# Performance work log

Hardware: AMD Instinct MI355X
Metric: run time of the kernel (lower is better)

The kernel has to match this reference:

```python
import math
import jax, jax.numpy as jnp
import numpy as np
from jax import lax

LEAKY_SLOPE = 0.2
ACT_GAIN = math.sqrt(2.0)

def bilinear_filter():
    h = jnp.array([1.0, 3.0, 3.0, 1.0], dtype=jnp.float32)
    h = h[:, None] * h[None, :]
    return h / jnp.sum(h)

def setup_inputs() -> dict:
    key = jax.random.key(0)
    ks = jax.random.split(key, 6)
    B, Cin, Cout, W_DIM, R = 16, 512, 512, 512, 64
    return {
        "x": jax.random.normal(ks[0], (B, Cin, R // 2, R // 2), dtype=jnp.float32),
        "w": jax.random.normal(ks[1], (B, W_DIM), dtype=jnp.float32),
        "noise_raw": jax.random.normal(ks[2], (B, 1, R, R), dtype=jnp.float32),
        "affine_weight": jax.random.normal(ks[3], (Cin, W_DIM), dtype=jnp.float32),
        "affine_bias": jnp.ones((Cin,), dtype=jnp.float32),
        "weight": jax.random.normal(ks[4], (Cout, Cin, 3, 3), dtype=jnp.float32),
        "bias": 0.1 * jax.random.normal(ks[5], (Cout,), dtype=jnp.float32),
        "noise_strength": jnp.float32(1.0),
    }

def reference(x, w, noise_raw, affine_weight, affine_bias, weight, bias, noise_strength):
    B, Cin = x.shape[0], x.shape[1]
    Cout = weight.shape[0]
    w_dim = affine_weight.shape[1]
    # EqualizedLinear affine: weight_gain = 1/sqrt(in), bias_gain = 1, no activation
    styles = w @ (affine_weight * (1.0 / math.sqrt(w_dim))).T + affine_bias  # [B, Cin]
    # demodulation coefficients from modulated weights
    wmod = weight[None] * styles[:, None, :, None, None]                      # [B,Cout,Cin,3,3]
    dcoefs = lax.rsqrt(jnp.sum(jnp.square(wmod), axis=(2, 3, 4)) + 1e-8)     # [B, Cout]
    # modulate input instead of weights
    xs = x * styles[:, :, None, None]
    # up=True path: conv_transpose2d(x, weight.transpose(0,1), stride=2, padding=0)
    # == dilated conv with spatially flipped kernel, pad k-1=2
    w_flip = weight[:, :, ::-1, ::-1]
    y = lax.conv_general_dilated(
        xs, w_flip, window_strides=(1, 1), padding=[(2, 2), (2, 2)],
        lhs_dilation=(2, 2), dimension_numbers=("NCHW", "OIHW", "NCHW"))    # [B,Cout,2H+1,2H+1]
    # filter2d with 4x4 bilinear kernel, gain=4, padding=1 (depthwise)
    f = bilinear_filter() * 4.0
    kd = jnp.tile(f[None, None], (Cout, 1, 1, 1))                            # [Cout,1,4,4]
    y = lax.conv_general_dilated(
        y, kd, window_strides=(1, 1), padding=[(1, 1), (1, 1)],
        dimension_numbers=("NCHW", "OIHW", "NCHW"), feature_group_count=Cout)  # [B,Cout,2H,2H]
    # addcmul: noise + y * dcoefs
    noise = noise_raw * noise_strength
    y = noise + y * dcoefs[:, :, None, None]
    # bias, act gain sqrt(2), leaky relu 0.2
    y = (y + bias[None, :, None, None]) * ACT_GAIN
    return jnp.where(y >= 0, y, LEAKY_SLOPE * y)
```

## Files before the change

### kernel.cpp

```cpp
#include <hip/hip_runtime.h>
#include <hip/hip_bf16.h>
#include <stdint.h>

typedef float f32x4 __attribute__((ext_vector_type(4)));
typedef __bf16 bf16x8 __attribute__((ext_vector_type(8)));

#define GLDS16(gp, lp) __builtin_amdgcn_global_load_lds( \
    (const __attribute__((address_space(1))) void*)(gp), \
    (__attribute__((address_space(3))) void*)(lp), 16, 0, 0)

static __device__ __forceinline__ unsigned short f2bf(float f) {
    unsigned int u = __float_as_uint(f);
    u = (u + 0x7fffu + ((u >> 16) & 1u)) >> 16;
    return (unsigned short)u;
}
static __device__ __forceinline__ float bf2f(unsigned short v) {
    return __uint_as_float(((unsigned int)v) << 16);
}

#define O_STYLES 0
#define O_DCOEF  32768
#define O_XS     65536
#define O_WP     19005440
#define O_Y1     23724032
#define O_WSQ    23724032
#define WS_NEED  96075776
#define SP 1104

__global__ __launch_bounds__(256) void k_styles(const float* __restrict__ w,
                                                const float* __restrict__ aw,
                                                const float* __restrict__ ab,
                                                float* __restrict__ styles) {
    int g = blockIdx.x * 256 + threadIdx.x;
    int b = g >> 9, ci = g & 511;
    const float4* wr = (const float4*)(w + b * 512);
    const float4* ar = (const float4*)(aw + ci * 512);
    float acc = 0.f;
    for (int k = 0; k < 128; ++k) {
        float4 wv = wr[k], av = ar[k];
        acc += wv.x * av.x + wv.y * av.y + wv.z * av.z + wv.w * av.w;
    }
    styles[g] = acc * 0.04419417382415922f + ab[ci];
}

__global__ __launch_bounds__(256) void k_wprep(const float* __restrict__ weight,
                                               float* __restrict__ wsq,
                                               unsigned short* __restrict__ wp) {
    int g = blockIdx.x * 256 + threadIdx.x;
    const float* wb = weight + (long)g * 9;
    float v[9]; float s = 0.f;
#pragma unroll
    for (int t = 0; t < 9; ++t) { v[t] = wb[t]; s += v[t] * v[t]; }
    wsq[g] = s;
    const int wri[9] = {2, 2, 0, 0, 2, 0, 1, 1, 1};
    const int wci[9] = {2, 0, 2, 0, 1, 1, 2, 0, 1};
#pragma unroll
    for (int t = 0; t < 9; ++t)
        wp[t * 262144 + g] = f2bf(v[wri[t] * 3 + wci[t]]);
}

__global__ __launch_bounds__(256) void k_dcoef(const float* __restrict__ styles,
                                               const float* __restrict__ wsq,
                                               float* __restrict__ dcoefs) {
    int g = blockIdx.x * 256 + threadIdx.x;
    int b = g >> 9, co = g & 511;
    const float4* sr = (const float4*)(styles + b * 512);
    const float4* qr = (const float4*)(wsq + co * 512);
    float acc = 1e-8f;
    for (int k = 0; k < 128; ++k) {
        float4 sv = sr[k], qv = qr[k];
        acc += sv.x * sv.x * qv.x + sv.y * sv.y * qv.y + sv.z * sv.z * qv.z + sv.w * sv.w * qv.w;
    }
    dcoefs[g] = rsqrtf(acc);
}

__global__ __launch_bounds__(256) void k_xprep(const float* __restrict__ x,
                                               const float* __restrict__ styles,
                                               unsigned short* __restrict__ xs) {
    __shared__ float T[128][33];
    int bid = blockIdx.x;
    int cc = bid & 3, i = (bid >> 2) & 31, b = bid >> 7;
    int t = threadIdx.x;
    int ci0 = cc * 128;
    int j_r = t & 31, cl_r = t >> 5;
    const float* xp = x + (((long)(b * 512 + ci0)) * 32 + i) * 32;
#pragma unroll
    for (int it = 0; it < 16; ++it) {
        int cl = cl_r + it * 8;
        T[cl][j_r] = xp[cl * 1024 + j_r];
    }
    __syncthreads();
    int ci_w = t & 127, jg = t >> 7;
    float sv = styles[b * 512 + ci0 + ci_w];
    unsigned short* op = xs + (((long)(b * 34 + (i + 1))) * 34 + 1) * 512 + ci0 + ci_w;
#pragma unroll
    for (int jj = 0; jj < 16; ++jj) {
        int j = jg * 16 + jj;
        op[(long)j * 512] = f2bf(T[ci_w][j] * sv);
    }
}

__global__ __launch_bounds__(256) void k_conv(const unsigned short* __restrict__ xs,
                                              const unsigned short* __restrict__ wp,
                                              unsigned short* __restrict__ y1) {
    __shared__ __align__(16) unsigned char lds[16384];
    int bid = (blockIdx.x & 7) * 288 + (blockIdx.x >> 3);
    int nt = bid & 3;
    int tmp = bid >> 2;
    int mt = tmp % 9;
    int tmp2 = tmp / 9;
    int par = tmp2 & 3, b = tmp2 >> 2;
    int tid = threadIdx.x;
    int wave = tid >> 6, lane = tid & 63;

    const int coff = (tid & 3) * 16;
    long abase0, abase1, bbase0, bbase1;
    {
        int row0 = tid >> 2;
        int gm0 = mt * 128 + row0;
        int r0 = gm0 / 33, s0 = gm0 % 33; if (r0 > 32) r0 = 32;
        int gm1 = gm0 + 64;
        int r1 = gm1 / 33, s1 = gm1 % 33; if (r1 > 32) r1 = 32;
        abase0 = (long)(((b * 34 + r0) * 34 + s0)) * 1024 + coff;
        abase1 = (long)(((b * 34 + r1) * 34 + s1)) * 1024 + coff;
        int co0 = nt * 128 + row0;
        bbase0 = (long)co0 * 1024 + coff;
        bbase1 = (long)(co0 + 64) * 1024 + coff;
    }
    const unsigned char* xsb = (const unsigned char*)xs;
    const unsigned char* wpb = (const unsigned char*)wp;

    int a_par = par >> 1, c_par = par & 1;
    int ntaps = a_par ? (c_par ? 1 : 2) : (c_par ? 2 : 4);
    int tapofs = (par == 0) ? 0 : ((par == 1) ? 4 : ((par == 2) ? 6 : 8));
    int KT = ntaps << 4;

    f32x4 acc[4][4];
#pragma unroll
    for (int mi = 0; mi < 4; ++mi)
#pragma unroll
        for (int ni = 0; ni < 4; ++ni)
            acc[mi][ni] = (f32x4){0.f, 0.f, 0.f, 0.f};

    int wr = wave >> 1, wc = wave & 1;
    int lrow = lane & 15;
    int lk = (lane >> 4) * 16;

    for (int kt = 0; kt < KT; ++kt) {
        int tl = kt >> 4, cib = kt & 15;
        int dio = a_par ? 1 : (c_par ? tl : (tl >> 1));
        int djo = c_par ? 1 : (a_par ? tl : (tl & 1));
        long dd = (long)dio * 34816 + (long)djo * 1024 + cib * 64;
        long wd = (long)(tapofs + tl) * 524288 + cib * 64;
        GLDS16(xsb + abase0 + dd, lds + wave * 1024);
        GLDS16(xsb + abase1 + dd, lds + 4096 + wave * 1024);
        GLDS16(wpb + bbase0 + wd, lds + 8192 + wave * 1024);
        GLDS16(wpb + bbase1 + wd, lds + 12288 + wave * 1024);
        __syncthreads();
        bf16x8 af[4], bfr[4];
#pragma unroll
        for (int mi = 0; mi < 4; ++mi)
            af[mi] = *(const bf16x8*)(lds + (wr * 64 + mi * 16 + lrow) * 64 + lk);
#pragma unroll
        for (int ni = 0; ni < 4; ++ni)
            bfr[ni] = *(const bf16x8*)(lds + 8192 + (wc * 64 + ni * 16 + lrow) * 64 + lk);
#pragma unroll
        for (int mi = 0; mi < 4; ++mi)
#pragma unroll
            for (int ni = 0; ni < 4; ++ni)
                acc[mi][ni] = __builtin_amdgcn_mfma_f32_16x16x32_bf16(af[mi], bfr[ni], acc[mi][ni], 0, 0, 0);
        __syncthreads();
    }

    long plane = (long)(b * 4 + par) * 512;
#pragma unroll
    for (int mi = 0; mi < 4; ++mi) {
        int gm0 = mt * 128 + wr * 64 + mi * 16 + (lane >> 4) * 4;
#pragma unroll
        for (int ni = 0; ni < 4; ++ni) {
            int co = nt * 128 + wc * 64 + ni * 16 + (lane & 15);
            unsigned short* dst = y1 + (plane + co) * SP + gm0;
            if (gm0 <= 1084) {
                ushort4 pk;
                pk.x = f2bf(acc[mi][ni][0]);
                pk.y = f2bf(acc[mi][ni][1]);
                pk.z = f2bf(acc[mi][ni][2]);
                pk.w = f2bf(acc[mi][ni][3]);
                *(ushort4*)dst = pk;
            } else if (gm0 == 1088) {
                dst[0] = f2bf(acc[mi][ni][0]);
            }
        }
    }
}

__global__ __launch_bounds__(256) void k_blur(const unsigned short* __restrict__ y1,
                                              const float* __restrict__ dcoefs,
                                              const float* __restrict__ bias,
                                              const float* __restrict__ noise,
                                              const float* __restrict__ nstr,
                                              float* __restrict__ out) {
    __shared__ float yl[67 * 69];
    int bid = blockIdx.x;
    int cg = bid & 63, b = bid >> 6;
    int t = threadIdx.x;
    int n = t & 63, mq = t >> 6;
    float ns = nstr[0];

    for (int i = t; i < 67 * 69; i += 256) yl[i] = 0.f;
    __syncthreads();

    const int Rv[4] = {33, 33, 32, 32};
    const int Sv[4] = {33, 32, 33, 32};
    const float* npb = noise + b * 4096;

    for (int cc = 0; cc < 8; ++cc) {
        int co = cg * 8 + cc;
#pragma unroll
        for (int pl = 0; pl < 4; ++pl) {
            int ap = pl >> 1, cq = pl & 1;
            const unsigned short* src = y1 + ((long)((b * 4 + pl) * 512 + co)) * SP;
            int rv = Rv[pl], sv = Sv[pl];
            for (int it = t; it < 273; it += 256) {
                int p0 = it * 4;
                ushort4 v = *(const ushort4*)(src + p0);
                unsigned short vv[4] = {v.x, v.y, v.z, v.w};
#pragma unroll
                for (int k = 0; k < 4; ++k) {
                    int p = p0 + k;
                    if (p < 1089) {
                        int r = p / 33;
                        int s = p - r * 33;
                        if (r < rv && s < sv)
                            yl[(2 * r + ap + 1) * 69 + (2 * s + cq + 1)] = bf2f(vv[k]);
                    }
                }
            }
        }
        __syncthreads();

        float dc = dcoefs[b * 512 + co];
        float bi = bias[co];
        int m0 = mq * 16;
        const float* r0p = &yl[(m0 - 1 + 1) * 69 + n];
        const float* r1p = r0p + 69;
        const float* r2p = r1p + 69;
        float t0 = (r0p[0] + r0p[3]) + 3.f * (r0p[1] + r0p[2]);
        float t1 = (r1p[0] + r1p[3]) + 3.f * (r1p[1] + r1p[2]);
        float t2 = (r2p[0] + r2p[3]) + 3.f * (r2p[1] + r2p[2]);
        float* ob = out + ((long)(b * 512 + co)) * 4096;
#pragma unroll
        for (int k = 0; k < 16; ++k) {
            int m = m0 + k;
            const float* rp = &yl[(m + 3) * 69 + n];
            float t3 = (rp[0] + rp[3]) + 3.f * (rp[1] + rp[2]);
            float acc = (t0 + t3) + 3.f * (t1 + t2);
            float val = npb[m * 64 + n] * ns + acc * (0.0625f * dc);
            val = (val + bi) * 1.41421356237309515f;
            ob[m * 64 + n] = (val >= 0.f) ? val : 0.2f * val;
            t0 = t1; t1 = t2; t2 = t3;
        }
        __syncthreads();
    }
}

extern "C" void kernel_launch(void* const* d_in, const int* in_sizes, int n_in,
                              void* d_out, int out_size, void* d_ws, size_t ws_size,
                              hipStream_t stream) {
    (void)in_sizes; (void)n_in; (void)out_size;
    if (ws_size < (size_t)WS_NEED) return;
    const float* x      = (const float*)d_in[0];
    const float* w      = (const float*)d_in[1];
    const float* noise  = (const float*)d_in[2];
    const float* aw     = (const float*)d_in[3];
    const float* ab     = (const float*)d_in[4];
    const float* weight = (const float*)d_in[5];
    const float* bias   = (const float*)d_in[6];
    const float* nstr   = (const float*)d_in[7];
    float* out = (float*)d_out;
    char* ws = (char*)d_ws;
    float* styles          = (float*)(ws + O_STYLES);
    float* dcoefs          = (float*)(ws + O_DCOEF);
    unsigned short* xs     = (unsigned short*)(ws + O_XS);
    unsigned short* wp     = (unsigned short*)(ws + O_WP);
    unsigned short* y1     = (unsigned short*)(ws + O_Y1);
    float* wsq             = (float*)(ws + O_WSQ);

    hipMemsetAsync(xs, 0, 18939904, stream);
    k_styles<<<32,   256, 0, stream>>>(w, aw, ab, styles);
    k_wprep <<<1024, 256, 0, stream>>>(weight, wsq, wp);
    k_dcoef <<<32,   256, 0, stream>>>(styles, wsq, dcoefs);
    k_xprep <<<2048, 256, 0, stream>>>(x, styles, xs);
    k_conv  <<<2304, 256, 0, stream>>>(xs, wp, y1);
    k_blur  <<<1024, 256, 0, stream>>>(y1, dcoefs, bias, noise, nstr, out);
}
```

Before: 222.2 us.

## Rewrite conv GEMM with 256x256 tiles, double-buffered LDS and swizzled loads

Replaces the 128x128-tile, single-buffered implicit-GEMM conv with a 512-thread kernel using 256x256 tiles that flattens batch into the M dimension. It adds a double-buffered 128KB dynamic LDS pipeline with vmcnt-controlled prefetch, an XOR-swizzled LDS layout to avoid bank conflicts, and split MFMA phases with setprio. The goal is to hide global-load latency and increase operand reuse. In exchange it uses more LDS and registers per block and launches far fewer blocks, which can hurt load balance across CUs.

```diff
diff --git a/kernel.cpp b/kernel.cpp
--- a/kernel.cpp
+++ b/kernel.cpp
@@ -100,95 +100,134 @@
     }
 }
 
-__global__ __launch_bounds__(256) void k_conv(const unsigned short* __restrict__ xs,
-                                              const unsigned short* __restrict__ wp,
-                                              unsigned short* __restrict__ y1) {
-    __shared__ __align__(16) unsigned char lds[16384];
-    int bid = (blockIdx.x & 7) * 288 + (blockIdx.x >> 3);
-    int nt = bid & 3;
-    int tmp = bid >> 2;
-    int mt = tmp % 9;
-    int tmp2 = tmp / 9;
-    int par = tmp2 & 3, b = tmp2 >> 2;
-    int tid = threadIdx.x;
-    int wave = tid >> 6, lane = tid & 63;
-
-    const int coff = (tid & 3) * 16;
-    long abase0, abase1, bbase0, bbase1;
-    {
-        int row0 = tid >> 2;
-        int gm0 = mt * 128 + row0;
-        int r0 = gm0 / 33, s0 = gm0 % 33; if (r0 > 32) r0 = 32;
-        int gm1 = gm0 + 64;
-        int r1 = gm1 / 33, s1 = gm1 % 33; if (r1 > 32) r1 = 32;
-        abase0 = (long)(((b * 34 + r0) * 34 + s0)) * 1024 + coff;
-        abase1 = (long)(((b * 34 + r1) * 34 + s1)) * 1024 + coff;
-        int co0 = nt * 128 + row0;
-        bbase0 = (long)co0 * 1024 + coff;
-        bbase1 = (long)(co0 + 64) * 1024 + coff;
-    }
-    const unsigned char* xsb = (const unsigned char*)xs;
-    const unsigned char* wpb = (const unsigned char*)wp;
-
+#define G4 asm volatile("s_waitcnt vmcnt(4)" ::: "memory");
+#define ST_A(kk) { GLDS16(xsB + sA0 + akt + (kk)*64, smp + nb + (kk)*16384 + t16); \
+                   GLDS16(xsB + sA1 + akt + (kk)*64, smp + nb + (kk)*16384 + t16 + 8192); }
+#define ST_B(kk) { GLDS16(wpB + sB0 + bkt + (kk)*64, smp + nb + 32768 + (kk)*16384 + t16); \
+                   GLDS16(wpB + sB1 + bkt + (kk)*64, smp + nb + 32768 + (kk)*16384 + t16 + 8192); }
+#define PHASE(kk, mh, RB, STG, GRD) { \
+  _Pragma("unroll") for (int i = 0; i < 4; ++i) \
+    av[i] = *(const bf16x8*)(smp + cb + (kk)*16384 + abase + ((mh)*64 + i*16)*64); \
+  if (RB) { _Pragma("unroll") for (int j = 0; j < 4; ++j) \
+    bv[j] = *(const bf16x8*)(smp + cb + (kk)*16384 + bbase + (j*16)*64); } \
+  STG; \
+  __builtin_amdgcn_sched_barrier(0); \
+  GRD \
+  __builtin_amdgcn_s_barrier(); \
+  asm volatile("s_waitcnt lgkmcnt(0)" ::: "memory"); \
+  __builtin_amdgcn_sched_barrier(0); \
+  __builtin_amdgcn_s_setprio(1); \
+  _Pragma("unroll") for (int i = 0; i < 4; ++i) \
+    _Pragma("unroll") for (int j = 0; j < 4; ++j) \
+      acc[(mh)*4 + i][j] = __builtin_amdgcn_mfma_f32_16x16x32_bf16(av[i], bv[j], acc[(mh)*4 + i][j], 0, 0, 0); \
+  __builtin_amdgcn_s_setprio(0); \
+  __builtin_amdgcn_s_barrier(); }
+
+__global__ __launch_bounds__(512, 2) void k_conv(const unsigned short* __restrict__ xs,
+                                                 const unsigned short* __restrict__ wp,
+                                                 unsigned short* __restrict__ y1) {
+    extern __shared__ __align__(16) char smem[];
+    const unsigned char* xsB = (const unsigned char*)xs;
+    const unsigned char* wpB = (const unsigned char*)wp;
+    char* smp = smem;
+
+    int bid = blockIdx.x;
+    int par, q;
+    if (bid < 138)      { par = 0; q = bid; }
+    else if (bid < 276) { par = 1; q = bid - 138; }
+    else if (bid < 414) { par = 2; q = bid - 276; }
+    else                { par = 3; q = bid - 414; }
+    int Mtile = q >> 1, Ntile = q & 1;
     int a_par = par >> 1, c_par = par & 1;
     int ntaps = a_par ? (c_par ? 1 : 2) : (c_par ? 2 : 4);
     int tapofs = (par == 0) ? 0 : ((par == 1) ? 4 : ((par == 2) ? 6 : 8));
-    int KT = ntaps << 4;
-
-    f32x4 acc[4][4];
-#pragma unroll
-    for (int mi = 0; mi < 4; ++mi)
-#pragma unroll
-        for (int ni = 0; ni < 4; ++ni)
-            acc[mi][ni] = (f32x4){0.f, 0.f, 0.f, 0.f};
-
-    int wr = wave >> 1, wc = wave & 1;
+    int NKT = ntaps << 3;
+
+    int tid = threadIdx.x;
+    int lane = tid & 63, wave = tid >> 6;
+    int wm = wave >> 2, wn = wave & 3;
     int lrow = lane & 15;
-    int lk = (lane >> 4) * 16;
-
-    for (int kt = 0; kt < KT; ++kt) {
-        int tl = kt >> 4, cib = kt & 15;
+    int rchunk = (((lane >> 4) ^ ((lrow >> 1) & 3)) << 4);
+    int abase = (wm * 128 + lrow) * 64 + rchunk;
+    int bbase = 32768 + (wn * 64 + lrow) * 64 + rchunk;
+
+    int srow = tid >> 2;
+    int schunk = (((tid & 3) ^ ((tid >> 3) & 3)) << 4);
+    int sA0, sA1;
+    {
+        unsigned gm = (unsigned)(Mtile * 256 + srow);
+        if (gm > 17471u) gm = 17471u;
+        unsigned b_ = gm / 1092u; unsigned pix = gm - b_ * 1092u;
+        unsigned r = pix / 33u; unsigned s = pix - r * 33u;
+        sA0 = (int)(((b_ * 34u + r) * 34u + s) << 10) + schunk;
+        gm = (unsigned)(Mtile * 256 + srow + 128);
+        if (gm > 17471u) gm = 17471u;
+        b_ = gm / 1092u; pix = gm - b_ * 1092u;
+        r = pix / 33u; s = pix - r * 33u;
+        sA1 = (int)(((b_ * 34u + r) * 34u + s) << 10) + schunk;
+    }
+    int sB0 = ((Ntile * 256 + srow) << 10) + schunk;
+    int sB1 = sB0 + (128 << 10);
+    int t16 = tid << 4;
+
+    f32x4 acc[8][4];
+#pragma unroll
+    for (int i = 0; i < 8; ++i)
+#pragma unroll
+        for (int j = 0; j < 4; ++j)
+            acc[i][j] = (f32x4){0.f, 0.f, 0.f, 0.f};
+    bf16x8 av[4], bv[4];
+
+    auto mkA = [&](int kt) -> int {
+        int tl = kt >> 3; if (tl >= ntaps) tl = ntaps - 1;
+        int cib = kt & 7;
         int dio = a_par ? 1 : (c_par ? tl : (tl >> 1));
         int djo = c_par ? 1 : (a_par ? tl : (tl & 1));
-        long dd = (long)dio * 34816 + (long)djo * 1024 + cib * 64;
-        long wd = (long)(tapofs + tl) * 524288 + cib * 64;
-        GLDS16(xsb + abase0 + dd, lds + wave * 1024);
-        GLDS16(xsb + abase1 + dd, lds + 4096 + wave * 1024);
-        GLDS16(wpb + bbase0 + wd, lds + 8192 + wave * 1024);
-        GLDS16(wpb + bbase1 + wd, lds + 12288 + wave * 1024);
-        __syncthreads();
-        bf16x8 af[4], bfr[4];
-#pragma unroll
-        for (int mi = 0; mi < 4; ++mi)
-            af[mi] = *(const bf16x8*)(lds + (wr * 64 + mi * 16 + lrow) * 64 + lk);
-#pragma unroll
-        for (int ni = 0; ni < 4; ++ni)
-            bfr[ni] = *(const bf16x8*)(lds + 8192 + (wc * 64 + ni * 16 + lrow) * 64 + lk);
-#pragma unroll
-        for (int mi = 0; mi < 4; ++mi)
-#pragma unroll
-            for (int ni = 0; ni < 4; ++ni)
-                acc[mi][ni] = __builtin_amdgcn_mfma_f32_16x16x32_bf16(af[mi], bfr[ni], acc[mi][ni], 0, 0, 0);
-        __syncthreads();
-    }
-
-    long plane = (long)(b * 4 + par) * 512;
-#pragma unroll
-    for (int mi = 0; mi < 4; ++mi) {
-        int gm0 = mt * 128 + wr * 64 + mi * 16 + (lane >> 4) * 4;
-#pragma unroll
-        for (int ni = 0; ni < 4; ++ni) {
-            int co = nt * 128 + wc * 64 + ni * 16 + (lane & 15);
-            unsigned short* dst = y1 + (plane + co) * SP + gm0;
-            if (gm0 <= 1084) {
+        return dio * 34816 + djo * 1024 + cib * 128;
+    };
+    auto mkB = [&](int kt) -> long {
+        int tl = kt >> 3; if (tl >= ntaps) tl = ntaps - 1;
+        return (long)(tapofs + tl) * 524288 + (long)((kt & 7) * 128);
+    };
+
+    {
+        int akt = mkA(0); long bkt = mkB(0); int nb = 0;
+        ST_A(0); ST_B(0); ST_A(1); ST_B(1);
+    }
+    __builtin_amdgcn_sched_barrier(0);
+    asm volatile("s_waitcnt vmcnt(4)" ::: "memory");
+    __builtin_amdgcn_s_barrier();
+
+    int cur = 0;
+    for (int kt = 0; kt < NKT; ++kt) {
+        int akt = mkA(kt + 1);
+        long bkt = mkB(kt + 1);
+        int nb = (cur ^ 1) << 16;
+        int cb = cur << 16;
+        PHASE(0, 0, 1, ST_A(0), )
+        PHASE(0, 1, 0, ST_B(0), G4)
+        PHASE(1, 0, 1, ST_A(1), )
+        PHASE(1, 1, 0, ST_B(1), G4)
+        cur ^= 1;
+    }
+
+#pragma unroll
+    for (int mf = 0; mf < 8; ++mf) {
+        int gm0 = Mtile * 256 + wm * 128 + mf * 16 + ((lane >> 4) << 2);
+        if (gm0 < 17472) {
+            unsigned ug = (unsigned)gm0;
+            unsigned bb = ug / 1092u;
+            int pix0 = (int)(ug - bb * 1092u);
+            long rowb = ((long)((bb * 4u + par) * 512) + 0) * SP;
+#pragma unroll
+            for (int nf = 0; nf < 4; ++nf) {
+                int co = Ntile * 256 + wn * 64 + nf * 16 + lrow;
                 ushort4 pk;
-                pk.x = f2bf(acc[mi][ni][0]);
-                pk.y = f2bf(acc[mi][ni][1]);
-                pk.z = f2bf(acc[mi][ni][2]);
-                pk.w = f2bf(acc[mi][ni][3]);
-                *(ushort4*)dst = pk;
-            } else if (gm0 == 1088) {
-                dst[0] = f2bf(acc[mi][ni][0]);
+                pk.x = f2bf(acc[mf][nf][0]);
+                pk.y = f2bf(acc[mf][nf][1]);
+                pk.z = f2bf(acc[mf][nf][2]);
+                pk.w = f2bf(acc[mf][nf][3]);
+                *(ushort4*)(y1 + rowb + (long)co * SP + pix0) = pk;
             }
         }
     }
@@ -254,8 +293,8 @@
             int m = m0 + k;
             const float* rp = &yl[(m + 3) * 69 + n];
             float t3 = (rp[0] + rp[3]) + 3.f * (rp[1] + rp[2]);
-            float acc = (t0 + t3) + 3.f * (t1 + t2);
-            float val = npb[m * 64 + n] * ns + acc * (0.0625f * dc);
+            float a = (t0 + t3) + 3.f * (t1 + t2);
+            float val = npb[m * 64 + n] * ns + a * (0.0625f * dc);
             val = (val + bi) * 1.41421356237309515f;
             ob[m * 64 + n] = (val >= 0.f) ? val : 0.2f * val;
             t0 = t1; t1 = t2; t2 = t3;
@@ -286,11 +325,14 @@
     unsigned short* y1     = (unsigned short*)(ws + O_Y1);
     float* wsq             = (float*)(ws + O_WSQ);
 
+    hipFuncSetAttribute((const void*)k_conv,
+                        hipFuncAttributeMaxDynamicSharedMemorySize, 131072);
+
     hipMemsetAsync(xs, 0, 18939904, stream);
     k_styles<<<32,   256, 0, stream>>>(w, aw, ab, styles);
     k_wprep <<<1024, 256, 0, stream>>>(weight, wsq, wp);
     k_dcoef <<<32,   256, 0, stream>>>(styles, wsq, dcoefs);
     k_xprep <<<2048, 256, 0, stream>>>(x, styles, xs);
-    k_conv  <<<2304, 256, 0, stream>>>(xs, wp, y1);
+    k_conv  <<<552,  512, 131072, stream>>>(xs, wp, y1);
     k_blur  <<<1024, 256, 0, stream>>>(y1, dcoefs, bias, noise, nstr, out);
 }
```

Result: faster. 212.7 us (-4.3%).
